# Optimization experiments

Measured on AMD Instinct MI355X. Metric: run time of the kernel, lower is better.

The kernel has to match this reference:

```python
import jax, jax.numpy as jnp
import numpy as np

B, S, F, H = 64, 2048, 1024, 1024


def setup_inputs() -> dict:
    key = jax.random.key(0)
    k0, k1, k2, k3, k4 = jax.random.split(key, 5)
    scale = 1.0 / np.sqrt(H)
    return {
        "inputs": jax.random.normal(k0, (B, S, F), jnp.float32),
        "hidden_state": jnp.zeros((B, H), jnp.float32),
        "W_ih": jax.random.uniform(k1, (H, F), jnp.float32, -scale, scale),
        "W_hh": jax.random.uniform(k2, (H, H), jnp.float32, -scale, scale),
        "b_ih": jax.random.uniform(k3, (H,), jnp.float32, -scale, scale),
        "b_hh": jax.random.uniform(k4, (H,), jnp.float32, -scale, scale),
        "chunk_len": 128,
        "chunk_stride": 128,
    }


def reference(inputs, hidden_state, W_ih, W_hh, b_ih, b_hh, chunk_len, chunk_stride):
    # ReverseRNNLayer with chunk_stride == chunk_len and S % chunk_len == 0:
    # each chunk starts from a zeroed hidden state (incl. the first chunk) and is
    # scanned in reverse time order; outputs are collected per index then the
    # whole list is reversed, yielding chunks in reverse chunk order with
    # ascending time order inside each chunk.
    b_, S_, F_ = inputs.shape
    H_ = W_hh.shape[0]
    L = chunk_len
    NC = S_ // L
    # (B, NC, L, F) -> reversed time within chunk -> (L, B*NC, F)
    xc = inputs.reshape(b_, NC, L, F_)
    xr = jnp.flip(xc, axis=2).transpose(2, 0, 1, 3).reshape(L, b_ * NC, F_)
    # precompute input projection outside the scan (hoists the big GEMM)
    xproj = xr @ W_ih.T + (b_ih + b_hh)  # (L, B*NC, H)

    def step(h, xp):
        h = jnp.tanh(xp + h @ W_hh.T)
        return h, h

    h0 = jnp.zeros((b_ * NC, H_), inputs.dtype)
    h_last, ys = jax.lax.scan(step, h0, xproj)  # ys: (L, B*NC, H), reversed time
    ys = jnp.flip(ys, axis=0)                   # ascending time within chunk
    ys = ys.reshape(L, b_, NC, H_).transpose(1, 2, 0, 3)  # (B, NC, L, H)
    ys = jnp.flip(ys, axis=1).reshape(b_, S_, H_)  # chunks in reverse chunk order
    # final hidden state = carry after processing the LAST chunk
    h_final = h_last.reshape(b_, NC, H_)[:, NC - 1]
    return ys, h_final
```

## Files before the change

kernel.cpp:

```cpp
#include <hip/hip_runtime.h>
#include <hip/hip_bf16.h>
#include <stdint.h>

typedef __bf16 bf16x8 __attribute__((ext_vector_type(8)));
typedef float f32x4 __attribute__((ext_vector_type(4)));

#define Bb 64
#define Ss 2048
#define Ff 1024
#define Hh 1024
#define Ll 128
#define NCc 16

__device__ __forceinline__ uint16_t f2bf_rne(float x) {
    union { float f; uint32_t u; } c; c.f = x;
    uint32_t u = c.u;
    return (uint16_t)((u + 0x7FFFu + ((u >> 16) & 1u)) >> 16);
}

__device__ __forceinline__ void load_lds16(const void* g, void* l) {
    __builtin_amdgcn_global_load_lds(
        (__attribute__((address_space(1))) void*)(uintptr_t)g,
        (__attribute__((address_space(3))) void*)l, 16, 0, 0);
}

__global__ __launch_bounds__(256) void prep_kernel(
    const float* __restrict__ Wih, const float* __restrict__ Whh,
    const float* __restrict__ bih, const float* __restrict__ bhh,
    uint16_t* __restrict__ wih_bf, uint16_t* __restrict__ whh_bf,
    uint16_t* __restrict__ h0, float* __restrict__ bias)
{
    int i = blockIdx.x * 256 + threadIdx.x;
    wih_bf[i] = f2bf_rne(Wih[i]);
    whh_bf[i] = f2bf_rne(Whh[i]);
    h0[i] = 0;
    if (i < Hh) bias[i] = bih[i] + bhh[i];
}

__global__ __launch_bounds__(256) void xproj_kernel(
    const float* __restrict__ x, const uint16_t* __restrict__ wih,
    const float* __restrict__ bias, float* __restrict__ out)
{
    __shared__ __bf16 As[128*32];
    __shared__ __bf16 Bs[128*32];
    const int hb = blockIdx.x, mb = blockIdx.y;
    const int tid = threadIdx.x;
    const int wave = tid >> 6, lane = tid & 63;
    const int wm = (wave >> 1) * 64, wn = (wave & 1) * 64;

    const int t  = mb >> 3;
    const int n0 = (mb & 7) * 128;

    int arow[4], acol[4];
#pragma unroll
    for (int p = 0; p < 4; ++p) {
        int idx = p*256 + tid;
        int r = idx >> 3, c4 = idx & 7;
        int n = n0 + r;
        int b = n >> 4, c = n & 15;
        arow[p] = b*Ss + c*Ll + (Ll-1-t);
        acol[p] = c4*4;
    }

    f32x4 acc[4][4] = {};

    for (int k0 = 0; k0 < Ff; k0 += 32) {
        __syncthreads();
#pragma unroll
        for (int p = 0; p < 2; ++p) {
            int idx = p*256 + tid;
            int r = idx >> 2, c = idx & 3;
            load_lds16(wih + (size_t)(hb*128 + r)*1024 + (k0 + c*8), (char*)Bs + idx*16);
        }
#pragma unroll
        for (int p = 0; p < 4; ++p) {
            int idx = p*256 + tid;
            const float4 v = *(const float4*)(x + (size_t)arow[p]*Ff + k0 + acol[p]);
            uint32_t lo = (uint32_t)f2bf_rne(v.x) | ((uint32_t)f2bf_rne(v.y) << 16);
            uint32_t hi = (uint32_t)f2bf_rne(v.z) | ((uint32_t)f2bf_rne(v.w) << 16);
            *(uint2*)((char*)As + idx*8) = make_uint2(lo, hi);
        }
        __syncthreads();

        bf16x8 af[4], bfr[4];
#pragma unroll
        for (int i = 0; i < 4; ++i)
            af[i] = *(const bf16x8*)&As[(wm + i*16 + (lane & 15))*32 + (lane >> 4)*8];
#pragma unroll
        for (int j = 0; j < 4; ++j)
            bfr[j] = *(const bf16x8*)&Bs[(wn + j*16 + (lane & 15))*32 + (lane >> 4)*8];
#pragma unroll
        for (int i = 0; i < 4; ++i)
#pragma unroll
            for (int j = 0; j < 4; ++j)
                acc[i][j] = __builtin_amdgcn_mfma_f32_16x16x32_bf16(af[i], bfr[j], acc[i][j], 0, 0, 0);
    }

    float bsv[4]; int coln[4];
#pragma unroll
    for (int j = 0; j < 4; ++j) {
        coln[j] = hb*128 + wn + j*16 + (lane & 15);
        bsv[j] = bias[coln[j]];
    }
#pragma unroll
    for (int i = 0; i < 4; ++i) {
#pragma unroll
        for (int r = 0; r < 4; ++r) {
            int n = n0 + wm + i*16 + (lane >> 4)*4 + r;
            int b = n >> 4, c = n & 15;
            size_t orow = (size_t)b*Ss + (size_t)(NCc-1-c)*Ll + (Ll-1-t);
            float* orp = out + orow*Hh;
#pragma unroll
            for (int j = 0; j < 4; ++j)
                orp[coln[j]] = acc[i][j][r] + bsv[j];
        }
    }
}

__global__ __launch_bounds__(256) void step_kernel(
    const uint16_t* __restrict__ hprev, uint16_t* __restrict__ hnext,
    const uint16_t* __restrict__ whh, float* __restrict__ out, int t)
{
    __shared__ __bf16 As[64*32];
    __shared__ __bf16 Bs[64*32];
    const int hb = blockIdx.x, nb = blockIdx.y;
    const int tid = threadIdx.x;
    const int wave = tid >> 6, lane = tid & 63;
    const int wm = (wave >> 1)*32, wn = (wave & 1)*32;

    const int sr = tid >> 2, sc = (tid & 3)*8;

    f32x4 acc[2][2] = {};

    for (int k0 = 0; k0 < Hh; k0 += 32) {
        __syncthreads();
        load_lds16(hprev + (size_t)(nb*64 + sr)*1024 + k0 + sc, (char*)As + tid*16);
        load_lds16(whh   + (size_t)(hb*64 + sr)*1024 + k0 + sc, (char*)Bs + tid*16);
        __syncthreads();

        bf16x8 af[2], bfr[2];
#pragma unroll
        for (int i = 0; i < 2; ++i)
            af[i] = *(const bf16x8*)&As[(wm + i*16 + (lane & 15))*32 + (lane >> 4)*8];
#pragma unroll
        for (int j = 0; j < 2; ++j)
            bfr[j] = *(const bf16x8*)&Bs[(wn + j*16 + (lane & 15))*32 + (lane >> 4)*8];
#pragma unroll
        for (int i = 0; i < 2; ++i)
#pragma unroll
            for (int j = 0; j < 2; ++j)
                acc[i][j] = __builtin_amdgcn_mfma_f32_16x16x32_bf16(af[i], bfr[j], acc[i][j], 0, 0, 0);
    }

#pragma unroll
    for (int i = 0; i < 2; ++i) {
#pragma unroll
        for (int r = 0; r < 4; ++r) {
            int n = nb*64 + wm + (lane >> 4)*4 + i*16 + r;
            int b = n >> 4, c = n & 15;
            size_t orow = (size_t)b*Ss + (size_t)(NCc-1-c)*Ll + (Ll-1-t);
            float* orp = out + orow*Hh;
            uint16_t* hnp = hnext + (size_t)n*Hh;
#pragma unroll
            for (int j = 0; j < 2; ++j) {
                int col = hb*64 + wn + j*16 + (lane & 15);
                float z = orp[col] + acc[i][j][r];
                float e = __expf(2.0f*z);
                float h = 1.0f - 2.0f/(e + 1.0f);
                orp[col] = h;
                hnp[col] = f2bf_rne(h);
            }
        }
    }
}

__global__ __launch_bounds__(256) void final_kernel(float* __restrict__ out) {
    int i = blockIdx.x*256 + threadIdx.x;
    int b = i >> 10, h = i & 1023;
    out[(size_t)Bb*Ss*Hh + i] = out[(size_t)b*Ss*Hh + h];
}

extern "C" void kernel_launch(void* const* d_in, const int* in_sizes, int n_in,
                              void* d_out, int out_size, void* d_ws, size_t ws_size,
                              hipStream_t stream)
{
    const float* x   = (const float*)d_in[0];
    const float* Wih = (const float*)d_in[2];
    const float* Whh = (const float*)d_in[3];
    const float* bih = (const float*)d_in[4];
    const float* bhh = (const float*)d_in[5];
    float* out = (float*)d_out;

    char* ws = (char*)d_ws;
    uint16_t* wih_bf = (uint16_t*)(ws);
    uint16_t* whh_bf = (uint16_t*)(ws + (size_t)(2<<20));
    uint16_t* hb0    = (uint16_t*)(ws + (size_t)(4<<20));
    uint16_t* hb1    = (uint16_t*)(ws + (size_t)(6<<20));
    float*    bias   = (float*)(ws + (size_t)(8<<20));

    prep_kernel<<<4096, 256, 0, stream>>>(Wih, Whh, bih, bhh, wih_bf, whh_bf, hb0, bias);
    xproj_kernel<<<dim3(8, 1024), 256, 0, stream>>>(x, wih_bf, bias, out);
    for (int t = 0; t < 128; ++t) {
        const uint16_t* hp = (t & 1) ? hb1 : hb0;
        uint16_t*       hn = (t & 1) ? hb0 : hb1;
        step_kernel<<<dim3(16, 16), 256, 0, stream>>>(hp, hn, whh_bf, out, t);
    }
    final_kernel<<<256, 256, 0, stream>>>(out);
}
```

Measured before the change: 3.422 ms.

## Replace per-step launches with persistent cooperative scan kernel using group barriers

The 128 per-timestep kernel launches become one persistent cooperative kernel. Each block keeps its 64-row slice of W_hh resident in LDS, streams h through a double-buffered swizzled LDS tile, and synchronises with the 16 blocks sharing its batch slice through a global atomic counter barrier. This removes launch overhead and the repeated W_hh reloads, and also writes the final hidden state inline and remaps the xproj grid. In exchange it relies on all 256 blocks being co-resident, uses large LDS per block (one block per CU), and adds spin-wait barrier latency on every step.

```diff
diff --git a/kernel.cpp b/kernel.cpp
--- a/kernel.cpp
+++ b/kernel.cpp
@@ -28,13 +28,15 @@
     const float* __restrict__ Wih, const float* __restrict__ Whh,
     const float* __restrict__ bih, const float* __restrict__ bhh,
     uint16_t* __restrict__ wih_bf, uint16_t* __restrict__ whh_bf,
-    uint16_t* __restrict__ h0, float* __restrict__ bias)
+    uint16_t* __restrict__ h0, float* __restrict__ bias,
+    unsigned* __restrict__ bar)
 {
     int i = blockIdx.x * 256 + threadIdx.x;
     wih_bf[i] = f2bf_rne(Wih[i]);
     whh_bf[i] = f2bf_rne(Whh[i]);
     h0[i] = 0;
     if (i < Hh) bias[i] = bih[i] + bhh[i];
+    if (i < 1024) bar[i] = 0u;
 }
 
 __global__ __launch_bounds__(256) void xproj_kernel(
@@ -43,7 +45,8 @@
 {
     __shared__ __bf16 As[128*32];
     __shared__ __bf16 Bs[128*32];
-    const int hb = blockIdx.x, mb = blockIdx.y;
+    const int hb = blockIdx.y & 7;
+    const int mb = blockIdx.x * 128 + (blockIdx.y >> 3);
     const int tid = threadIdx.x;
     const int wave = tid >> 6, lane = tid & 63;
     const int wm = (wave >> 1) * 64, wn = (wave & 1) * 64;
@@ -117,67 +120,148 @@
     }
 }
 
-__global__ __launch_bounds__(256) void step_kernel(
-    const uint16_t* __restrict__ hprev, uint16_t* __restrict__ hnext,
-    const uint16_t* __restrict__ whh, float* __restrict__ out, int t)
-{
-    __shared__ __bf16 As[64*32];
-    __shared__ __bf16 Bs[64*32];
-    const int hb = blockIdx.x, nb = blockIdx.y;
+
+__device__ __forceinline__ void stage_A(const uint16_t* __restrict__ hp, int nb, int c,
+                                        __bf16* dst, int tid) {
+#pragma unroll
+    for (int p = 0; p < 2; ++p) {
+        int u = p*256 + tid;
+        int r = u >> 3;
+        int s = u & 7;
+        int k = (c << 6) + ((s ^ (r & 7)) << 3);
+        load_lds16(hp + ((size_t)(nb*64 + r) << 10) + k, (char*)dst + u*16);
+    }
+}
+
+__global__ __launch_bounds__(256, 1) void scan_kernel(
+    const uint16_t* __restrict__ whh,
+    uint16_t* __restrict__ h0buf, uint16_t* __restrict__ h1buf,
+    float* __restrict__ out, unsigned* __restrict__ bar)
+{
+    __shared__ __align__(16) __bf16 Bs[64 * 1024];
+    __shared__ __align__(16) __bf16 As[2][64 * 64];
+
+    const int bid = blockIdx.x;
+    const int nb = bid & 15;
+    const int hb = bid >> 4;
     const int tid = threadIdx.x;
-    const int wave = tid >> 6, lane = tid & 63;
-    const int wm = (wave >> 1)*32, wn = (wave & 1)*32;
-
-    const int sr = tid >> 2, sc = (tid & 3)*8;
-
-    f32x4 acc[2][2] = {};
-
-    for (int k0 = 0; k0 < Hh; k0 += 32) {
-        __syncthreads();
-        load_lds16(hprev + (size_t)(nb*64 + sr)*1024 + k0 + sc, (char*)As + tid*16);
-        load_lds16(whh   + (size_t)(hb*64 + sr)*1024 + k0 + sc, (char*)Bs + tid*16);
-        __syncthreads();
-
-        bf16x8 af[2], bfr[2];
+    const int lane = tid & 63;
+    const int wave = tid >> 6;
+    const int wm = (wave >> 1) * 32, wn = (wave & 1) * 32;
+    const int l15 = lane & 15, l4 = lane >> 4;
+
+    unsigned* cnt = bar + nb * 64;
+    unsigned* gen = bar + nb * 64 + 32;
+
+    for (int u = tid; u < 8192; u += 256) {
+        int r = u >> 7, s = u & 127;
+        int k = (s ^ (r & 7)) << 3;
+        bf16x8 v = *(const bf16x8*)(whh + ((size_t)(hb*64 + r) << 10) + k);
+        *(bf16x8*)((char*)Bs + u*16) = v;
+    }
+
+    float* orb[2][4];
+    int hoff[2][4];
+#pragma unroll
+    for (int i = 0; i < 2; ++i)
+#pragma unroll
+        for (int r = 0; r < 4; ++r) {
+            int n = nb*64 + wm + l4*4 + i*16 + r;
+            int b = n >> 4, cch = n & 15;
+            orb[i][r] = out + ((size_t)b*Ss + (size_t)(NCc-1-cch)*Ll)*Hh + hb*64;
+            hoff[i][r] = n*Hh + hb*64;
+        }
+
+    __syncthreads();
+
+#pragma unroll 1
+    for (int t = 0; t < Ll; ++t) {
+        const uint16_t* hp = (t & 1) ? h1buf : h0buf;
+        uint16_t*       hn = (t & 1) ? h0buf : h1buf;
+        const size_t toff = (size_t)(Ll-1-t) * Hh;
+
+        float xpv[2][4][2];
 #pragma unroll
         for (int i = 0; i < 2; ++i)
-            af[i] = *(const bf16x8*)&As[(wm + i*16 + (lane & 15))*32 + (lane >> 4)*8];
-#pragma unroll
-        for (int j = 0; j < 2; ++j)
-            bfr[j] = *(const bf16x8*)&Bs[(wn + j*16 + (lane & 15))*32 + (lane >> 4)*8];
+#pragma unroll
+            for (int r = 0; r < 4; ++r) {
+                const float* orp = orb[i][r] + toff;
+                xpv[i][r][0] = orp[wn + l15];
+                xpv[i][r][1] = orp[wn + 16 + l15];
+            }
+
+        f32x4 acc[2][2] = {};
+
+        if (t > 0) {
+            stage_A(hp, nb, 0, &As[0][0], tid);
+            __syncthreads();
+#pragma unroll
+            for (int c = 0; c < 16; ++c) {
+                if (c < 15) stage_A(hp, nb, c + 1, &As[(c + 1) & 1][0], tid);
+                const char* Ab = (const char*)&As[c & 1][0];
+#pragma unroll
+                for (int ks = 0; ks < 2; ++ks) {
+                    bf16x8 af[2], bv[2];
+#pragma unroll
+                    for (int i = 0; i < 2; ++i) {
+                        int r = wm + i*16 + l15;
+                        int off = r*128 + ((ks*64 + l4*16) ^ ((r & 7) << 4));
+                        af[i] = *(const bf16x8*)(Ab + off);
+                    }
+#pragma unroll
+                    for (int j = 0; j < 2; ++j) {
+                        int r = wn + j*16 + l15;
+                        int off = r*2048 + ((c*128 + ks*64 + l4*16) ^ ((r & 7) << 4));
+                        bv[j] = *(const bf16x8*)((const char*)Bs + off);
+                    }
+#pragma unroll
+                    for (int i = 0; i < 2; ++i)
+#pragma unroll
+                        for (int j = 0; j < 2; ++j)
+                            acc[i][j] = __builtin_amdgcn_mfma_f32_16x16x32_bf16(af[i], bv[j], acc[i][j], 0, 0, 0);
+                }
+                __syncthreads();
+            }
+        }
+
 #pragma unroll
         for (int i = 0; i < 2; ++i)
 #pragma unroll
-            for (int j = 0; j < 2; ++j)
-                acc[i][j] = __builtin_amdgcn_mfma_f32_16x16x32_bf16(af[i], bfr[j], acc[i][j], 0, 0, 0);
-    }
-
-#pragma unroll
-    for (int i = 0; i < 2; ++i) {
-#pragma unroll
-        for (int r = 0; r < 4; ++r) {
-            int n = nb*64 + wm + (lane >> 4)*4 + i*16 + r;
-            int b = n >> 4, c = n & 15;
-            size_t orow = (size_t)b*Ss + (size_t)(NCc-1-c)*Ll + (Ll-1-t);
-            float* orp = out + orow*Hh;
-            uint16_t* hnp = hnext + (size_t)n*Hh;
-#pragma unroll
-            for (int j = 0; j < 2; ++j) {
-                int col = hb*64 + wn + j*16 + (lane & 15);
-                float z = orp[col] + acc[i][j][r];
-                float e = __expf(2.0f*z);
-                float h = 1.0f - 2.0f/(e + 1.0f);
-                orp[col] = h;
-                hnp[col] = f2bf_rne(h);
-            }
-        }
-    }
-}
-
-__global__ __launch_bounds__(256) void final_kernel(float* __restrict__ out) {
-    int i = blockIdx.x*256 + threadIdx.x;
-    int b = i >> 10, h = i & 1023;
-    out[(size_t)Bb*Ss*Hh + i] = out[(size_t)b*Ss*Hh + h];
+            for (int r = 0; r < 4; ++r) {
+                float* orp = orb[i][r] + toff;
+                uint16_t* hnp = hn + hoff[i][r];
+#pragma unroll
+                for (int j = 0; j < 2; ++j) {
+                    int colo = wn + j*16 + l15;
+                    float z = xpv[i][r][j] + acc[i][j][r];
+                    float e = __expf(2.0f*z);
+                    float h = 1.0f - 2.0f/(e + 1.0f);
+                    orp[colo] = h;
+                    hnp[colo] = f2bf_rne(h);
+                    if (t == Ll-1 && r == 3 && l4 == 3) {
+                        int b = (nb*64 + wm + i*16 + 15) >> 4;
+                        out[(size_t)Bb*Ss*Hh + (size_t)b*Hh + hb*64 + colo] = h;
+                    }
+                }
+            }
+
+        if (t < Ll - 1) {
+            __syncthreads();
+            if (tid == 0) {
+                unsigned g = __hip_atomic_load(gen, __ATOMIC_RELAXED, __HIP_MEMORY_SCOPE_AGENT);
+                unsigned a = __hip_atomic_fetch_add(cnt, 1u, __ATOMIC_ACQ_REL, __HIP_MEMORY_SCOPE_AGENT);
+                if (a == 15u) {
+                    __hip_atomic_store(cnt, 0u, __ATOMIC_RELAXED, __HIP_MEMORY_SCOPE_AGENT);
+                    __hip_atomic_store(gen, g + 1u, __ATOMIC_RELEASE, __HIP_MEMORY_SCOPE_AGENT);
+                } else {
+                    while (__hip_atomic_load(gen, __ATOMIC_RELAXED, __HIP_MEMORY_SCOPE_AGENT) == g)
+                        __builtin_amdgcn_s_sleep(2);
+                    (void)__hip_atomic_load(gen, __ATOMIC_ACQUIRE, __HIP_MEMORY_SCOPE_AGENT);
+                }
+            }
+            __syncthreads();
+        }
+    }
 }
 
 extern "C" void kernel_launch(void* const* d_in, const int* in_sizes, int n_in,
@@ -197,13 +281,11 @@
     uint16_t* hb0    = (uint16_t*)(ws + (size_t)(4<<20));
     uint16_t* hb1    = (uint16_t*)(ws + (size_t)(6<<20));
     float*    bias   = (float*)(ws + (size_t)(8<<20));
-
-    prep_kernel<<<4096, 256, 0, stream>>>(Wih, Whh, bih, bhh, wih_bf, whh_bf, hb0, bias);
+    unsigned* bar    = (unsigned*)(ws + (size_t)(8<<20) + 4096);
+
+    prep_kernel<<<4096, 256, 0, stream>>>(Wih, Whh, bih, bhh, wih_bf, whh_bf, hb0, bias, bar);
     xproj_kernel<<<dim3(8, 1024), 256, 0, stream>>>(x, wih_bf, bias, out);
-    for (int t = 0; t < 128; ++t) {
-        const uint16_t* hp = (t & 1) ? hb1 : hb0;
-        uint16_t*       hn = (t & 1) ? hb0 : hb1;
-        step_kernel<<<dim3(16, 16), 256, 0, stream>>>(hp, hn, whh_bf, out, t);
-    }
-    final_kernel<<<256, 256, 0, stream>>>(out);
-}
+
+    void* args[] = { (void*)&whh_bf, (void*)&hb0, (void*)&hb1, (void*)&out, (void*)&bar };
+    hipLaunchCooperativeKernel(scan_kernel, dim3(256), dim3(256), args, 0, stream);
+}
```

After: 3.436 ms. About the same (+0.4%).
